# Optimization experiments

Measured on AMD Instinct MI355X. Metric: run time of the kernel, lower is better.

Reference implementation:

```python
import jax, jax.numpy as jnp
import numpy as np

LN_EPS = 1e-5  # torch nn.LayerNorm default


def setup_inputs() -> dict:
    key = jax.random.key(0)
    ks = jax.random.split(key, 5)
    B, N, K, H, D = 1, 16384, 16, 4, 32
    q = jax.random.normal(ks[0], (B, N, H, D), dtype=jnp.float32)
    k_neigh = jax.random.normal(ks[1], (B, N, K, H, D), dtype=jnp.float32)
    v_neigh = jax.random.normal(ks[2], (B, N, K, H, D), dtype=jnp.float32)
    geo_f = jax.random.normal(ks[3], (B, N, K, D), dtype=jnp.float32)
    W = jax.random.normal(ks[4], (D, D), dtype=jnp.float32) * (1.0 / np.sqrt(D))
    b = jnp.zeros((D,), dtype=jnp.float32)
    ln_gamma = jnp.ones((D,), dtype=jnp.float32)
    ln_beta = jnp.zeros((D,), dtype=jnp.float32)
    return {"q": q, "k_neigh": k_neigh, "v_neigh": v_neigh, "geo_f": geo_f,
            "W": W, "b": b, "ln_gamma": ln_gamma, "ln_beta": ln_beta}


def reference(q, k_neigh, v_neigh, geo_f, W, b, ln_gamma, ln_beta):
    # q: [B,N,H,D], k_neigh/v_neigh: [B,N,K,H,D], geo_f: [B,N,K,D]
    scale = q.shape[-1] ** (-0.5)
    # broadcasted edge tensor [B,N,K,H,D]
    w = (q[:, :, None, :, :] - k_neigh + geo_f[:, :, :, None, :]) / scale
    # Linear(hdim,hdim) + ReLU + LayerNorm(hdim)
    w = jnp.einsum('bnkhd,ed->bnkhe', w, W) + b
    w = jax.nn.relu(w)
    mu = jnp.mean(w, axis=-1, keepdims=True)
    var = jnp.mean(jnp.square(w - mu), axis=-1, keepdims=True)
    w = (w - mu) * jax.lax.rsqrt(var + LN_EPS) * ln_gamma + ln_beta
    # subtract detached per-neighbor max (shift-invariant for softmax)
    w = w - jax.lax.stop_gradient(jnp.max(w, axis=2, keepdims=True))
    attn = jax.nn.softmax(w, axis=2)  # softmax over K neighbors
    # dropout p=0.0 -> identity
    out = jnp.sum(attn * v_neigh, axis=2)  # [B,N,H,D]
    return out
```

## Files before the change

kernel.cpp:

```cpp
#include <hip/hip_runtime.h>
#include <hip/hip_bf16.h>

constexpr int KNB = 16;
constexpr int HH  = 4;
constexpr int DD  = 32;
constexpr int NPB = 32;
constexpr int NBUF = 3;

typedef __attribute__((ext_vector_type(4))) float f32x4;
typedef __attribute__((ext_vector_type(8))) short bf16x8;
union BFRAG { bf16x8 v; unsigned u[4]; };

constexpr int L_K  = 0;
constexpr int L_V  = 2048;
constexpr int L_G  = 4096;
constexpr int L_Q  = 4608;
constexpr int L_SZ = 4864;

__device__ __forceinline__ unsigned pk_bf16(float a, float b) {
    union { __hip_bfloat162 b2; unsigned u; } r;
    r.b2 = __float22bfloat162_rn(make_float2(a, b));
    return r.u;
}
__device__ __forceinline__ float2 unpk_bf16(unsigned u) {
    union { unsigned u; __hip_bfloat162 b2; } r; r.u = u;
    return make_float2(__bfloat162float(r.b2.x), __bfloat162float(r.b2.y));
}
__device__ __forceinline__ void gload16(const float* g, float* l) {
    __builtin_amdgcn_global_load_lds(
        (const __attribute__((address_space(1))) unsigned*)g,
        (__attribute__((address_space(3))) unsigned*)l, 16, 0, 0);
}
__device__ __forceinline__ float dpp_x1(float x) {
    int s = __builtin_bit_cast(int, x);
    return __builtin_bit_cast(float,
        __builtin_amdgcn_update_dpp(s, s, 0xB1, 0xF, 0xF, false));
}
__device__ __forceinline__ float dpp_x2(float x) {
    int s = __builtin_bit_cast(int, x);
    return __builtin_bit_cast(float,
        __builtin_amdgcn_update_dpp(s, s, 0x4E, 0xF, 0xF, false));
}

__global__ __launch_bounds__(256, 2) void geoneigh_deep(
    const float* __restrict__ q, const float* __restrict__ kn,
    const float* __restrict__ vn, const float* __restrict__ geo,
    const float* __restrict__ W, const float* __restrict__ bvec,
    const float* __restrict__ gamma, const float* __restrict__ beta,
    float* __restrict__ out, int BN)
{
    __shared__ __align__(16) float lds[NBUF * L_SZ];

    const int tid = threadIdx.x;
    const int l   = tid & 63;
    const int wv  = tid >> 6;
    const int lm  = l & 15;
    const int lg  = l >> 4;

    const float SC    = 5.656854249492381f;
    const float LOG2E = 1.4426950408889634f;

    BFRAG Wh[2], Wl[2];
    #pragma unroll
    for (int t = 0; t < 2; ++t) {
        const float* wr = &W[(t * 16 + lm) * DD + lg * 8];
        const float4 wa = *(const float4*)wr;
        const float4 wb = *(const float4*)(wr + 4);
        float wf[8] = {wa.x * SC, wa.y * SC, wa.z * SC, wa.w * SC,
                       wb.x * SC, wb.y * SC, wb.z * SC, wb.w * SC};
        #pragma unroll
        for (int p = 0; p < 4; ++p) {
            const unsigned h = pk_bf16(wf[2 * p], wf[2 * p + 1]);
            const float2 hr = unpk_bf16(h);
            Wh[t].u[p] = h;
            Wl[t].u[p] = pk_bf16(wf[2 * p] - hr.x, wf[2 * p + 1] - hr.y);
        }
    }
    float bias[2], gamL[2], betL[2];
    #pragma unroll
    for (int t = 0; t < 2; ++t) {
        bias[t] = bvec[lm + 16 * t];
        gamL[t] = gamma[lm + 16 * t] * LOG2E;
        betL[t] = beta[lm + 16 * t] * LOG2E;
    }

    const int koff0 = lm * 128 + wv * 32 + lg * 8;
    const int voff  = ((l >> 2) & 3) * 512 + wv * 128
                    + ((l >> 4) & 3) * 32 + (l & 3) * 4;
    const int goff  = lm * 32 + lg * 8 + (wv & 1) * 4;
    const int qoff  = (l & 31) * 4;
    const int dK = L_K + wv * 512;
    const int dV = L_V + wv * 512;
    const int dG = L_G + (wv & 1) * 256;

    const int nbase = blockIdx.x * NPB;
    const int nmax  = BN - 1;

    auto stage = [&](int buf, int n) {
        const float* kN = kn  + (size_t)n * (KNB * HH * DD);
        const float* vN = vn  + (size_t)n * (KNB * HH * DD);
        const float* gN = geo + (size_t)n * (KNB * DD);
        const float* qN = q   + (size_t)n * (HH * DD);
        float* B = &lds[buf * L_SZ];
        gload16(kN + koff0,      B + dK);
        gload16(kN + koff0 + 4,  B + dK + 256);
        gload16(vN + voff,       B + dV);
        gload16(vN + voff + 16,  B + dV + 256);
        gload16(gN + goff,       B + dG);
        gload16(qN + qoff,       B + L_Q);
        __builtin_amdgcn_sched_barrier(0);
    };
    auto cnode = [&](int t) { int n = nbase + t; return n > nmax ? nmax : n; };

    stage(0, cnode(0));
    stage(1, cnode(1));

    int cb = 0, sb = 2;
    for (int t = 0; t < NPB; ++t) {
        stage(sb, cnode(t + 2));
        asm volatile("s_waitcnt vmcnt(12)" ::: "memory");
        __builtin_amdgcn_s_barrier();
        __builtin_amdgcn_sched_barrier(0);

        const float* B = &lds[cb * L_SZ];
        const int n = cnode(t);

        const f32x4 kf0 = *(const f32x4*)(B + L_K + wv * 512 + l * 4);
        const f32x4 kf1 = *(const f32x4*)(B + L_K + wv * 512 + 256 + l * 4);
        const f32x4 gf0 = *(const f32x4*)(B + L_G + l * 4);
        const f32x4 gf1 = *(const f32x4*)(B + L_G + 256 + l * 4);
        const f32x4 qf0 = *(const f32x4*)(B + L_Q + wv * 32 + lg * 8);
        const f32x4 qf1 = *(const f32x4*)(B + L_Q + wv * 32 + lg * 8 + 4);
        float vr[2][4];
        #pragma unroll
        for (int t2 = 0; t2 < 2; ++t2)
            #pragma unroll
            for (int r = 0; r < 4; ++r)
                vr[t2][r] = B[L_V + (r * 2 + t2) * 256 + wv * 64 + l];

        float wvv[8];
        #pragma unroll
        for (int j = 0; j < 4; ++j) {
            wvv[j]     = qf0[j] - kf0[j] + gf0[j];
            wvv[4 + j] = qf1[j] - kf1[j] + gf1[j];
        }
        BFRAG Ah, Al;
        #pragma unroll
        for (int p = 0; p < 4; ++p) {
            const unsigned h = pk_bf16(wvv[2 * p], wvv[2 * p + 1]);
            const float2 hr = unpk_bf16(h);
            Ah.u[p] = h;
            Al.u[p] = pk_bf16(wvv[2 * p] - hr.x, wvv[2 * p + 1] - hr.y);
        }
        f32x4 acc[2];
        #pragma unroll
        for (int t2 = 0; t2 < 2; ++t2) {
            f32x4 c = {bias[t2], bias[t2], bias[t2], bias[t2]};
            c = __builtin_amdgcn_mfma_f32_16x16x32_bf16(Ah.v, Wh[t2].v, c, 0, 0, 0);
            c = __builtin_amdgcn_mfma_f32_16x16x32_bf16(Ah.v, Wl[t2].v, c, 0, 0, 0);
            c = __builtin_amdgcn_mfma_f32_16x16x32_bf16(Al.v, Wh[t2].v, c, 0, 0, 0);
            acc[t2] = c;
        }

        float x[2][4], t1[4], t2s[4];
        #pragma unroll
        for (int t2 = 0; t2 < 2; ++t2)
            #pragma unroll
            for (int r = 0; r < 4; ++r)
                x[t2][r] = fmaxf(acc[t2][r], 0.f);
        #pragma unroll
        for (int r = 0; r < 4; ++r) {
            t1[r]  = x[0][r] + x[1][r];
            t2s[r] = x[0][r] * x[0][r] + x[1][r] * x[1][r];
        }
        #pragma unroll
        for (int r = 0; r < 4; ++r) {
            t1[r]  += dpp_x1(t1[r]);   t2s[r] += dpp_x1(t2s[r]);
            t1[r]  += dpp_x2(t1[r]);   t2s[r] += dpp_x2(t2s[r]);
            t1[r]  += __shfl_xor(t1[r], 4);  t2s[r] += __shfl_xor(t2s[r], 4);
            t1[r]  += __shfl_xor(t1[r], 8);  t2s[r] += __shfl_xor(t2s[r], 8);
        }
        float z[2][4];
        #pragma unroll
        for (int r = 0; r < 4; ++r) {
            const float mu  = t1[r] * 0.03125f;
            const float var = fmaxf(t2s[r] * 0.03125f - mu * mu, 0.f);
            const float inv = rsqrtf(var + 1e-5f);
            #pragma unroll
            for (int t2 = 0; t2 < 2; ++t2)
                z[t2][r] = (x[t2][r] - mu) * inv * gamL[t2] + betL[t2];
        }
        float S[2], o[2];
        #pragma unroll
        for (int t2 = 0; t2 < 2; ++t2) {
            float s = 0.f, oo = 0.f;
            #pragma unroll
            for (int r = 0; r < 4; ++r) {
                const float p = exp2f(z[t2][r]);
                s += p;
                oo = fmaf(p, vr[t2][r], oo);
            }
            s  += __shfl_xor(s, 16);
            s  += __shfl_xor(s, 32);
            oo += __shfl_xor(oo, 16);
            oo += __shfl_xor(oo, 32);
            S[t2] = s; o[t2] = oo;
        }
        if (l < 32) {
            const int sel = (l >> 4) & 1;
            const float oo = sel ? o[1] : o[0];
            const float ss = sel ? S[1] : S[0];
            out[((size_t)n * HH + wv) * DD + l] = __fdividef(oo, ss);
        }

        asm volatile("s_waitcnt lgkmcnt(0)" ::: "memory");
        __builtin_amdgcn_s_barrier();
        cb = (cb == NBUF - 1) ? 0 : cb + 1;
        sb = (sb == NBUF - 1) ? 0 : sb + 1;
    }
}

extern "C" void kernel_launch(void* const* d_in, const int* in_sizes, int n_in,
                              void* d_out, int out_size, void* d_ws, size_t ws_size,
                              hipStream_t stream) {
    const float* q   = (const float*)d_in[0];
    const float* kn  = (const float*)d_in[1];
    const float* vn  = (const float*)d_in[2];
    const float* geo = (const float*)d_in[3];
    const float* W   = (const float*)d_in[4];
    const float* b   = (const float*)d_in[5];
    const float* gam = (const float*)d_in[6];
    const float* bet = (const float*)d_in[7];
    float* out = (float*)d_out;

    const int BN     = in_sizes[0] / (HH * DD);
    const int blocks = (BN + NPB - 1) / NPB;

    hipLaunchKernelGGL(geoneigh_deep, dim3(blocks), dim3(256), 0, stream,
                       q, kn, vn, geo, W, b, gam, bet, out, BN);
}
```

Before: 71.34 us.

## Coalesce global-to-LDS staging with XOR-swizzled layout and fewer loads

```diff
diff --git a/kernel.cpp b/kernel.cpp
--- a/kernel.cpp
+++ b/kernel.cpp
@@ -15,7 +15,8 @@
 constexpr int L_V  = 2048;
 constexpr int L_G  = 4096;
 constexpr int L_Q  = 4608;
-constexpr int L_SZ = 4864;
+constexpr int L_P  = 4864;
+constexpr int L_SZ = 5120;
 
 __device__ __forceinline__ unsigned pk_bf16(float a, float b) {
     union { __hip_bfloat162 b2; unsigned u; } r;
@@ -42,7 +43,7 @@
         __builtin_amdgcn_update_dpp(s, s, 0x4E, 0xF, 0xF, false));
 }
 
-__global__ __launch_bounds__(256, 2) void geoneigh_deep(
+__global__ __launch_bounds__(256, 2) void geoneigh_coal(
     const float* __restrict__ q, const float* __restrict__ kn,
     const float* __restrict__ vn, const float* __restrict__ geo,
     const float* __restrict__ W, const float* __restrict__ bvec,
@@ -84,14 +85,39 @@
         betL[t] = beta[lm + 16 * t] * LOG2E;
     }
 
-    const int koff0 = lm * 128 + wv * 32 + lg * 8;
-    const int voff  = ((l >> 2) & 3) * 512 + wv * 128
-                    + ((l >> 4) & 3) * 32 + (l & 3) * 4;
-    const int goff  = lm * 32 + lg * 8 + (wv & 1) * 4;
-    const int qoff  = (l & 31) * 4;
-    const int dK = L_K + wv * 512;
-    const int dV = L_V + wv * 512;
-    const int dG = L_G + (wv & 1) * 256;
+    int srcKV[2], dstKV[2];
+    #pragma unroll
+    for (int j = 0; j < 2; ++j) {
+        const int row = 4 * wv + 2 * j + (l >> 5);
+        srcKV[j] = row * 128 + ((((l & 31) ^ (row & 7))) << 2);
+        dstKV[j] = (2 * wv + j) * 256;
+    }
+    int src5, dst5;
+    if (wv < 2) {
+        const int j2  = wv * 64 + l;
+        const int row = j2 >> 3;
+        src5 = row * 32 + (((j2 & 7) ^ (row & 7)) << 2);
+        dst5 = L_G + wv * 256;
+    } else {
+        src5 = (l & 31) * 4;
+        dst5 = (wv == 2) ? L_Q : L_P;
+    }
+
+    const int kO0 = L_K + lm * 128 + (((wv * 8 + lg * 2 + 0) ^ (lm & 7)) << 2);
+    const int kO1 = L_K + lm * 128 + (((wv * 8 + lg * 2 + 1) ^ (lm & 7)) << 2);
+    const int gO0 = L_G + lm * 32  + ((((lg * 2 + 0) ^ (lm & 7))) << 2);
+    const int gO1 = L_G + lm * 32  + ((((lg * 2 + 1) ^ (lm & 7))) << 2);
+    const int qO0 = L_Q + wv * 32 + lg * 8;
+    int vO[2][4];
+    #pragma unroll
+    for (int t2 = 0; t2 < 2; ++t2)
+        #pragma unroll
+        for (int r = 0; r < 4; ++r) {
+            const int row = lg * 4 + r;
+            vO[t2][r] = L_V + row * 128 +
+                        (((wv * 8 + t2 * 4 + (lm >> 2)) ^ (row & 7)) << 2) +
+                        (lm & 3);
+        }
 
     const int nbase = blockIdx.x * NPB;
     const int nmax  = BN - 1;
@@ -99,16 +125,14 @@
     auto stage = [&](int buf, int n) {
         const float* kN = kn  + (size_t)n * (KNB * HH * DD);
         const float* vN = vn  + (size_t)n * (KNB * HH * DD);
-        const float* gN = geo + (size_t)n * (KNB * DD);
-        const float* qN = q   + (size_t)n * (HH * DD);
         float* B = &lds[buf * L_SZ];
-        gload16(kN + koff0,      B + dK);
-        gload16(kN + koff0 + 4,  B + dK + 256);
-        gload16(vN + voff,       B + dV);
-        gload16(vN + voff + 16,  B + dV + 256);
-        gload16(gN + goff,       B + dG);
-        gload16(qN + qoff,       B + L_Q);
-        __builtin_amdgcn_sched_barrier(0);
+        gload16(kN + srcKV[0], B + L_K + dstKV[0]);
+        gload16(kN + srcKV[1], B + L_K + dstKV[1]);
+        gload16(vN + srcKV[0], B + L_V + dstKV[0]);
+        gload16(vN + srcKV[1], B + L_V + dstKV[1]);
+        const float* b5 = (wv < 2) ? geo + (size_t)n * (KNB * DD)
+                                   : q   + (size_t)n * (HH * DD);
+        gload16(b5 + src5, B + dst5);
     };
     auto cnode = [&](int t) { int n = nbase + t; return n > nmax ? nmax : n; };
 
@@ -118,25 +142,25 @@
     int cb = 0, sb = 2;
     for (int t = 0; t < NPB; ++t) {
         stage(sb, cnode(t + 2));
-        asm volatile("s_waitcnt vmcnt(12)" ::: "memory");
+        asm volatile("s_waitcnt vmcnt(10)" ::: "memory");
         __builtin_amdgcn_s_barrier();
         __builtin_amdgcn_sched_barrier(0);
 
         const float* B = &lds[cb * L_SZ];
         const int n = cnode(t);
 
-        const f32x4 kf0 = *(const f32x4*)(B + L_K + wv * 512 + l * 4);
-        const f32x4 kf1 = *(const f32x4*)(B + L_K + wv * 512 + 256 + l * 4);
-        const f32x4 gf0 = *(const f32x4*)(B + L_G + l * 4);
-        const f32x4 gf1 = *(const f32x4*)(B + L_G + 256 + l * 4);
-        const f32x4 qf0 = *(const f32x4*)(B + L_Q + wv * 32 + lg * 8);
-        const f32x4 qf1 = *(const f32x4*)(B + L_Q + wv * 32 + lg * 8 + 4);
+        const f32x4 kf0 = *(const f32x4*)(B + kO0);
+        const f32x4 kf1 = *(const f32x4*)(B + kO1);
+        const f32x4 gf0 = *(const f32x4*)(B + gO0);
+        const f32x4 gf1 = *(const f32x4*)(B + gO1);
+        const f32x4 qf0 = *(const f32x4*)(B + qO0);
+        const f32x4 qf1 = *(const f32x4*)(B + qO0 + 4);
         float vr[2][4];
         #pragma unroll
         for (int t2 = 0; t2 < 2; ++t2)
             #pragma unroll
             for (int r = 0; r < 4; ++r)
-                vr[t2][r] = B[L_V + (r * 2 + t2) * 256 + wv * 64 + l];
+                vr[t2][r] = B[vO[t2][r]];
 
         float wvv[8];
         #pragma unroll
@@ -236,6 +260,6 @@
     const int BN     = in_sizes[0] / (HH * DD);
     const int blocks = (BN + NPB - 1) / NPB;
 
-    hipLaunchKernelGGL(geoneigh_deep, dim3(blocks), dim3(256), 0, stream,
+    hipLaunchKernelGGL(geoneigh_coal, dim3(blocks), dim3(256), 0, stream,
                        q, kn, vn, geo, W, b, gam, bet, out, BN);
 }
```

Result: no change. 72.16 us (+1.1%).
